# Kernel tuning notes

Measured on AMD Instinct MI355X. Metric: run time of the kernel, lower is better.

The kernel has to match this reference:

```python
import jax, jax.numpy as jnp
import numpy as np

# LIFParameters(thr=0.4, tau=20.0, tau_o=20.0, damp=0.3, n_ref=5)
THR = 0.4
DECAY = float(np.exp(-1.0 / 20.0))   # membrane decay
KAPPA = float(np.exp(-1.0 / 20.0))   # output filter decay
N_REF = 5.0
DAMP = 0.3
SCALE = 1.0                           # scaling_factor

B, NIN, H, NOUT = 1024, 2048, 2048, 512


def setup_inputs() -> dict:
    key = jax.random.key(0)
    ks = jax.random.split(key, 10)
    inputs = (jax.random.uniform(ks[0], (B, NIN)) < 0.1).astype(jnp.float32)   # input spikes
    v = jax.random.uniform(ks[1], (B, H)) * THR                                # membrane potentials
    z = (jax.random.uniform(ks[2], (B, H)) < 0.2).astype(jnp.float32)          # previous spikes
    r = jax.random.randint(ks[3], (B, H), 0, 6).astype(jnp.float32)            # refractory counters
    out = jax.random.normal(ks[4], (B, NOUT)) * 0.1                            # filtered output
    trace_in = jax.random.uniform(ks[5], (B, NIN))
    trace_rec = jax.random.uniform(ks[6], (B, H))
    w_in = jax.random.normal(ks[7], (NIN, H)) / np.sqrt(NIN)
    w_rec = jax.random.normal(ks[8], (H, H)) / np.sqrt(H)
    w_out = jax.random.normal(ks[9], (H, NOUT)) / np.sqrt(H)
    return dict(inputs=inputs, v=v, z=z, r=r, out=out, trace_in=trace_in,
                trace_rec=trace_rec, w_in=w_in, w_rec=w_rec, w_out=w_out)


@jax.custom_vjp
def spike(v_scaled):
    return (v_scaled > 0.0).astype(v_scaled.dtype)

def _spike_fwd(v_scaled):
    return spike(v_scaled), v_scaled

def _spike_bwd(v_scaled, g):
    # surrogate gradient: damp * max(0, 1 - |v_scaled|)
    return (g * DAMP * jnp.maximum(1.0 - jnp.abs(v_scaled), 0.0),)

spike.defvjp(_spike_fwd, _spike_bwd)


def reference(inputs, v, z, r, out, trace_in, trace_rec, w_in, w_rec, w_out):
    # --- lif_step ---
    i_t = inputs @ w_in + z @ w_rec                      # [B,H] synaptic current
    new_v = DECAY * v + i_t - z * THR                    # leaky integration + reset
    v_scaled = (new_v - THR) / THR
    new_z = spike(v_scaled)
    new_z = jnp.where(r > 0.1, 0.0, new_z)               # refractory masking (old r)
    new_r = jnp.clip(r + N_REF * new_z - 1.0, 0.0, N_REF)
    new_out = KAPPA * out + new_z @ (w_out * SCALE)      # [B,NOUT]
    # --- e-prop extras (call_eprop) ---
    dz_dh = jnp.maximum(DAMP * (1.0 - jnp.abs(v_scaled)), 0.0) / THR
    dz_dh = jnp.where(r > 0.1, 0.0, dz_dh)               # zero in refractory period
    new_trace_in = trace_in * DECAY + inputs
    new_trace_rec = trace_rec * DECAY + z
    return (new_out, new_z, new_v, new_r, new_trace_in, new_trace_rec, dz_dh)
```

## Files before the change

### kernel.cpp

```cpp
#include <hip/hip_runtime.h>

#define Bq 1024
#define Hq 2048
#define NOUTq 512

#define DECAYF 0.95122942450071400910f
#define THRF 0.4f
#define SINVF 5931641.0f

#define OFF_OUT  0
#define OFF_Z    524288
#define OFF_V    2621440
#define OFF_R    4718592
#define OFF_TIN  6815744
#define OFF_TREC 8912896
#define OFF_DZ   11010048

#define WS_A     0ul
#define WS_Q0    4194304ul
#define WS_Q1    12582912ul
#define WS_Q2    20971520ul
#define WS_WOUTT 29360128ul
#define WS_P     31457280ul
#define WS_Z2    65011712ul
#define WS_NEED  69206016ul

typedef __attribute__((ext_vector_type(8))) short  bf16x8;
typedef __attribute__((ext_vector_type(4))) short  s16x4;
typedef __attribute__((ext_vector_type(4))) float  f32x4;
typedef __attribute__((ext_vector_type(4))) int    i32x4;
typedef __attribute__((ext_vector_type(4))) char   c8x4;

#define VMCNT8  asm volatile("s_waitcnt vmcnt(8)" ::: "memory")
#define VMCNT0  asm volatile("s_waitcnt vmcnt(0)" ::: "memory")
#define LGKM0   asm volatile("s_waitcnt lgkmcnt(0)" ::: "memory")
#define SB0     __builtin_amdgcn_sched_barrier(0)
#define BARRAW  __builtin_amdgcn_s_barrier()

__device__ __forceinline__ unsigned short cvt_bf16(float f) {
  unsigned u = __float_as_uint(f);
  return (unsigned short)((u + 0x7FFFu + ((u >> 16) & 1u)) >> 16);
}

__device__ __forceinline__ void gl_lds16(const void* g, void* l) {
  __builtin_amdgcn_global_load_lds((const __attribute__((address_space(1))) unsigned int*)g,
                                   (__attribute__((address_space(3))) unsigned int*)l, 16, 0, 0);
}


__global__ __launch_bounds__(256)
void prep(const float* __restrict__ w_in, const float* __restrict__ w_rec,
          const float* __restrict__ w_out, signed char* __restrict__ Q0,
          signed char* __restrict__ Q1, signed char* __restrict__ Q2,
          short* __restrict__ WoutT,
          const f32x4* __restrict__ ins, const f32x4* __restrict__ zin,
          signed char* __restrict__ Acomb)
{
  __shared__ float tile[64][65];
  const int bx = blockIdx.x, tid = threadIdx.x;
  if (bx >= 2304) {
    const int i = (bx - 2304) * 256 + tid;
    const f32x4 b = ins[i];
    const f32x4 d = zin[i];
    const int e = i * 4, m = e >> 11, k = e & 2047;
    c8x4 ab, zb;
#pragma unroll
    for (int j = 0; j < 4; ++j) { ab[j] = (char)(b[j] != 0.0f); zb[j] = (char)(d[j] != 0.0f); }
    *(c8x4*)&Acomb[m * 4096 + k] = ab;
    *(c8x4*)&Acomb[m * 4096 + 2048 + k] = zb;
    return;
  }
  const int rr = tid >> 4, c4 = (tid & 15) * 4;
  if (bx < 2048) {
    const int k0 = (bx >> 5) * 64, n0 = (bx & 31) * 64;
#pragma unroll
    for (int p = 0; p < 4; ++p) {
      const int kk = p * 16 + rr, kg = k0 + kk;
      const float* src = (kg < 2048) ? &w_in[kg * 2048 + n0 + c4]
                                     : &w_rec[(kg - 2048) * 2048 + n0 + c4];
      const f32x4 v = *(const f32x4*)src;
#pragma unroll
      for (int j = 0; j < 4; ++j) tile[kk][c4 + j] = v[j];
    }
    __syncthreads();
#pragma unroll
    for (int p = 0; p < 4; ++p) {
      const int nn = p * 16 + rr;
      c8x4 b0, b1, b2;
#pragma unroll
      for (int j = 0; j < 4; ++j) {
        int q = __float2int_rn(tile[c4 + j][nn] * SINVF);
        const int d2 = ((q + 64) & 127) - 64;  q = (q - d2) >> 7;
        const int d1 = ((q + 64) & 127) - 64;  q = (q - d1) >> 7;
        b2[j] = (char)d2; b1[j] = (char)d1; b0[j] = (char)q;
      }
      const long off = (long)(n0 + nn) * 4096 + k0 + c4;
      *(c8x4*)&Q0[off] = b0;
      *(c8x4*)&Q1[off] = b1;
      *(c8x4*)&Q2[off] = b2;
    }
  } else {
    const int b2 = bx - 2048;
    const int k0 = (b2 >> 3) * 64, n0 = (b2 & 7) * 64;
#pragma unroll
    for (int p = 0; p < 4; ++p) {
      const int kk = p * 16 + rr;
      const f32x4 v = *(const f32x4*)&w_out[(k0 + kk) * 512 + n0 + c4];
#pragma unroll
      for (int j = 0; j < 4; ++j) tile[kk][c4 + j] = v[j];
    }
    __syncthreads();
#pragma unroll
    for (int p = 0; p < 4; ++p) {
      const int nn = p * 16 + rr;
      s16x4 hh;
#pragma unroll
      for (int j = 0; j < 4; ++j) hh[j] = (short)cvt_bf16(tile[c4 + j][nn]);
      *(s16x4*)&WoutT[(n0 + nn) * 2048 + k0 + c4] = hh;
    }
  }
}

__global__ __launch_bounds__(512, 1)
void gemm1(const signed char* __restrict__ Ag, const signed char* __restrict__ Q0g,
           const signed char* __restrict__ Q1g, const signed char* __restrict__ Q2g,
           int* __restrict__ outp)
{
  constexpr int KT = 8;
  __shared__ __align__(16) signed char L[2][4][16384];

  const int tid = threadIdx.x, lane = tid & 63, wv = tid >> 6;
  const int lr = lane & 15, hl = lane >> 4;
  const int r8 = lane >> 3, ts = lane & 7;

  const int bid = blockIdx.x;
  const int swz = (bid & 7) * 64 + (bid >> 3);
  const int m0 = (swz & 7) * 128;
  const int n0 = ((swz >> 3) & 15) * 128;
  const int kz = swz >> 7;
  const int kb = kz * 1024;
  int* P = outp + (size_t)kz * (Bq * Hq);

  const int wm = (wv & 3) * 32;
  const int wn = (wv >> 2) * 64;

  i32x4 a0[2][4], a1[2][4], a2[2][4];
#pragma unroll
  for (int mi = 0; mi < 2; ++mi)
#pragma unroll
    for (int ni = 0; ni < 4; ++ni) {
      a0[mi][ni] = (i32x4){0, 0, 0, 0};
      a1[mi][ni] = (i32x4){0, 0, 0, 0};
      a2[mi][ni] = (i32x4){0, 0, 0, 0};
    }

  auto STAGE = [&](int kt, int c) {
    const int k = kb + kt * 128;
#pragma unroll
    for (int q = 0; q < 2; ++q) {
      const int slot = wv * 2 + q;
      const int r = slot * 8 + r8;
      const int s = ts ^ (r & 7);
      const size_t go = (size_t)r * 4096 + k + s * 16;
      gl_lds16(Ag  + (size_t)m0 * 4096 + go, &L[c][0][slot * 1024]);
      gl_lds16(Q0g + (size_t)n0 * 4096 + go, &L[c][1][slot * 1024]);
      gl_lds16(Q1g + (size_t)n0 * 4096 + go, &L[c][2][slot * 1024]);
      gl_lds16(Q2g + (size_t)n0 * 4096 + go, &L[c][3][slot * 1024]);
    }
  };

  auto COMPUTE = [&](int c) {
#pragma unroll
    for (int ks = 0; ks < 2; ++ks) {
      i32x4 af[2];
#pragma unroll
      for (int mi = 0; mi < 2; ++mi) {
        const int ar = wm + mi * 16 + lr;
        af[mi] = *(const i32x4*)&L[c][0][ar * 128 + (((ks * 4 + hl) ^ (ar & 7)) << 4)];
      }
#pragma unroll
      for (int ni = 0; ni < 4; ++ni) {
        const int br = wn + ni * 16 + lr;
        const int sp = br * 128 + (((ks * 4 + hl) ^ (br & 7)) << 4);
        const i32x4 b0 = *(const i32x4*)&L[c][1][sp];
#pragma unroll
        for (int mi = 0; mi < 2; ++mi)
          a0[mi][ni] = __builtin_amdgcn_mfma_i32_16x16x64_i8(af[mi], b0, a0[mi][ni], 0, 0, 0);
        const i32x4 b1 = *(const i32x4*)&L[c][2][sp];
#pragma unroll
        for (int mi = 0; mi < 2; ++mi)
          a1[mi][ni] = __builtin_amdgcn_mfma_i32_16x16x64_i8(af[mi], b1, a1[mi][ni], 0, 0, 0);
        const i32x4 b2 = *(const i32x4*)&L[c][3][sp];
#pragma unroll
        for (int mi = 0; mi < 2; ++mi)
          a2[mi][ni] = __builtin_amdgcn_mfma_i32_16x16x64_i8(af[mi], b2, a2[mi][ni], 0, 0, 0);
      }
    }
  };

  STAGE(0, 0);
  STAGE(1, 1);
  for (int kt = 0; kt < KT - 1; ++kt) {
    VMCNT8; SB0; BARRAW; SB0;
    COMPUTE(kt & 1);
    LGKM0; SB0; BARRAW; SB0;
    if (kt + 2 < KT) STAGE(kt + 2, kt & 1);
  }
  VMCNT0; SB0; BARRAW; SB0;
  COMPUTE((KT - 1) & 1);

#pragma unroll
  for (int mi = 0; mi < 2; ++mi)
#pragma unroll
    for (int ni = 0; ni < 4; ++ni)
#pragma unroll
      for (int j = 0; j < 4; ++j) {
        const int m = m0 + wm + mi * 16 + hl * 4 + j;
        const int n = n0 + wn + ni * 16 + lr;
        P[m * Hq + n] = (a0[mi][ni][j] << 14) + (a1[mi][ni][j] << 7) + a2[mi][ni][j];
      }
}

__global__ __launch_bounds__(256)
void lif_epi(const i32x4* __restrict__ Pp, const f32x4* __restrict__ vin,
             const f32x4* __restrict__ zin, const f32x4* __restrict__ rin,
             float* __restrict__ dout, short* __restrict__ z2)
{
  const int i = blockIdx.x * 256 + threadIdx.x;
  const i32x4 c = Pp[i] + Pp[i + 524288] + Pp[i + 2 * 524288] + Pp[i + 3 * 524288];
  const double S = 1.0 / (double)SINVF;
  const f32x4 vo = vin[i], zo = zin[i], ro = rin[i];
  f32x4 nv, nz, nr, dz;
  s16x4 zb;
#pragma unroll
  for (int j = 0; j < 4; ++j) {
    const float it = (float)((double)c[j] * S);
    const float v1 = DECAYF * vo[j] + it - zo[j] * THRF;
    const float vs = (v1 - THRF) / THRF;
    const bool refr = ro[j] > 0.1f;
    const float z1 = (refr || !(vs > 0.0f)) ? 0.0f : 1.0f;
    nv[j] = v1; nz[j] = z1;
    nr[j] = fminf(fmaxf(ro[j] + 5.0f * z1 - 1.0f, 0.0f), 5.0f);
    dz[j] = refr ? 0.0f : (fmaxf(0.3f * (1.0f - fabsf(vs)), 0.0f) / THRF);
    zb[j] = (short)cvt_bf16(z1);
  }
  ((f32x4*)(dout + OFF_V))[i] = nv;
  ((f32x4*)(dout + OFF_Z))[i] = nz;
  ((f32x4*)(dout + OFF_R))[i] = nr;
  ((f32x4*)(dout + OFF_DZ))[i] = dz;
  ((s16x4*)z2)[i] = zb;
}

__global__ __launch_bounds__(256)
void tail(const short* __restrict__ Ag, const short* __restrict__ Whg,
          const float* __restrict__ e0, float* __restrict__ outp,
          const f32x4* __restrict__ tin, const f32x4* __restrict__ ins,
          const f32x4* __restrict__ trec, const f32x4* __restrict__ zin,
          f32x4* __restrict__ o1, f32x4* __restrict__ o2)
{
  constexpr int BM = 32, BN = 64, MR = 1, NR = 2, KT = 32, AK = 2048;
  constexpr int APW = BM / 32, WPW = BN / 32;
  __shared__ __align__(16) short As[BM * 64];
  __shared__ __align__(16) short Wh[BN * 64];

  const int bid = blockIdx.x, tid = threadIdx.x;
  if (bid >= 256) {
    const int i = (bid - 256) * 256 + tid;
    o1[i] = tin[i] * DECAYF + ins[i];
    o2[i] = trec[i] * DECAYF + zin[i];
    return;
  }
  const int lane = tid & 63, wv = tid >> 6;
  const int lr = lane & 15, hl = lane >> 4;
  const int rA = lane >> 3, ts = lane & 7;
  const int m0 = (bid >> 3) * BM, n0 = (bid & 7) * BN;
  const int wm = (wv >> 1) * (MR * 16);
  const int wn = (wv & 1) * (NR * 16);

  f32x4 acc[MR][NR];
#pragma unroll
  for (int mi = 0; mi < MR; ++mi)
#pragma unroll
    for (int ni = 0; ni < NR; ++ni) acc[mi][ni] = (f32x4){0.f, 0.f, 0.f, 0.f};

  auto STAGE = [&](int kt) {
    const int k = kt * 64;
#pragma unroll
    for (int q = 0; q < APW; ++q) {
      const int slot = wv * APW + q;
      const int r = slot * 8 + rA;
      const int s = ts ^ (r & 7);
      gl_lds16(Ag + (m0 + r) * AK + k + s * 8, &As[slot * 512]);
    }
#pragma unroll
    for (int q = 0; q < WPW; ++q) {
      const int slot = wv * WPW + q;
      const int r = slot * 8 + rA;
      const int s = ts ^ (r & 7);
      gl_lds16(Whg + (n0 + r) * AK + k + s * 8, &Wh[slot * 512]);
    }
  };

  STAGE(0);
  for (int kt = 0; kt < KT; ++kt) {
    __syncthreads();
#pragma unroll
    for (int ks = 0; ks < 2; ++ks) {
      bf16x8 af[MR];
#pragma unroll
      for (int mi = 0; mi < MR; ++mi) {
        const int r = wm + mi * 16 + lr;
        af[mi] = *(const bf16x8*)&As[r * 64 + (((ks * 4 + hl) ^ (r & 7)) << 3)];
      }
#pragma unroll
      for (int ni = 0; ni < NR; ++ni) {
        const int rn = wn + ni * 16 + lr;
        const int sp = (((ks * 4 + hl) ^ (rn & 7)) << 3);
        const bf16x8 bh = *(const bf16x8*)&Wh[rn * 64 + sp];
#pragma unroll
        for (int mi = 0; mi < MR; ++mi)
          acc[mi][ni] = __builtin_amdgcn_mfma_f32_16x16x32_bf16(af[mi], bh, acc[mi][ni], 0, 0, 0);
      }
    }
    __syncthreads();
    if (kt + 1 < KT) STAGE(kt + 1);
  }

#pragma unroll
  for (int mi = 0; mi < MR; ++mi)
#pragma unroll
    for (int ni = 0; ni < NR; ++ni)
#pragma unroll
      for (int j = 0; j < 4; ++j) {
        const int m = m0 + wm + mi * 16 + hl * 4 + j;
        const int n = n0 + wn + ni * 16 + lr;
        const int idx = m * NOUTq + n;
        outp[idx] = DECAYF * e0[idx] + acc[mi][ni][j];
      }
}


template<int MODE>
__global__ __launch_bounds__(256, 1)
void fb_gemm(const float* __restrict__ A0g, const float* __restrict__ A1g,
             const float* __restrict__ W0g, const float* __restrict__ W1g,
             const float* __restrict__ e0, const float* __restrict__ e1,
             const float* __restrict__ e2, float* __restrict__ dout)
{
  constexpr int BM = (MODE == 0) ? 64 : 32;
  constexpr int BN = (MODE == 0) ? 128 : 64;
  constexpr int BK = 64;
  constexpr int LDA = BK + 8;
  constexpr int MR = (MODE == 0) ? 2 : 1;
  constexpr int NR = (MODE == 0) ? 4 : 2;
  constexpr int WM = MR * 16, WN = NR * 16;
  constexpr int KT = (MODE == 0) ? 64 : 32;
  constexpr int Nmat = (MODE == 0) ? Hq : NOUTq;
  constexpr int QA = BM / 16;
  constexpr int QW = (16 * BN) / 256;
  constexpr int KSH = (MODE == 0) ? 7 : 6;
  constexpr int KSTEP = (MODE == 0) ? 2 : 4;

  __shared__ __align__(16) short As[BM * LDA];
  __shared__ __align__(16) short Wh[BN * LDA];
  __shared__ __align__(16) short Wl[((MODE == 0) ? BN : 1) * LDA];

  const int tid  = threadIdx.x;
  const int lane = tid & 63;
  const int wave = tid >> 6;
  const int lr = lane & 15, hl = lane >> 4;
  const int wmOff = (wave >> 1) * WM;
  const int wnOff = (wave & 1) * WN;
  const int m0 = blockIdx.y * BM;
  const int n0 = blockIdx.x * BN;
  const int arow = tid >> 4, ac4 = tid & 15;
  const int wn = tid & (BN - 1);

  f32x4 aR[QA];
  float wR[QW][4];
  f32x4 acc[MR][NR];
#pragma unroll
  for (int mi = 0; mi < MR; ++mi)
#pragma unroll
    for (int ni = 0; ni < NR; ++ni)
      acc[mi][ni] = (f32x4){0.f, 0.f, 0.f, 0.f};

  auto LOAD = [&](int kt) {
    const float* Ag = A0g; const float* Wg = W0g; int k0 = kt * BK;
    if (MODE == 0 && kt >= 32) { Ag = A1g; Wg = W1g; k0 = (kt - 32) * BK; }
#pragma unroll
    for (int q = 0; q < QA; ++q)
      aR[q] = *(const f32x4*)&Ag[(m0 + arow + q * 16) * 2048 + k0 + ac4 * 4];
#pragma unroll
    for (int p = 0; p < QW; ++p) {
      const int kq = (tid >> KSH) + p * KSTEP;
#pragma unroll
      for (int i = 0; i < 4; ++i)
        wR[p][i] = Wg[(k0 + kq * 4 + i) * Nmat + n0 + wn];
    }
  };

  auto STORE = [&]() {
#pragma unroll
    for (int q = 0; q < QA; ++q) {
      s16x4 hv;
#pragma unroll
      for (int j = 0; j < 4; ++j) hv[j] = (short)cvt_bf16(aR[q][j]);
      *(s16x4*)&As[(arow + q * 16) * LDA + ac4 * 4] = hv;
    }
#pragma unroll
    for (int p = 0; p < QW; ++p) {
      const int kq = (tid >> KSH) + p * KSTEP;
      s16x4 hh, ll;
#pragma unroll
      for (int i = 0; i < 4; ++i) {
        const float w = wR[p][i];
        const unsigned short h = cvt_bf16(w);
        hh[i] = (short)h;
        if (MODE == 0) {
          const float hf = __uint_as_float(((unsigned)h) << 16);
          ll[i] = (short)cvt_bf16(w - hf);
        }
      }
      *(s16x4*)&Wh[wn * LDA + kq * 4] = hh;
      if (MODE == 0) *(s16x4*)&Wl[wn * LDA + kq * 4] = ll;
    }
  };

  LOAD(0);
  for (int kt = 0; kt < KT; ++kt) {
    __syncthreads();
    STORE();
    __syncthreads();
    if (kt + 1 < KT) LOAD(kt + 1);
#pragma unroll
    for (int ks = 0; ks < 2; ++ks) {
      bf16x8 af[MR];
#pragma unroll
      for (int mi = 0; mi < MR; ++mi)
        af[mi] = *(const bf16x8*)&As[(wmOff + mi * 16 + lr) * LDA + ks * 32 + hl * 8];
#pragma unroll
      for (int ni = 0; ni < NR; ++ni) {
        const bf16x8 bh = *(const bf16x8*)&Wh[(wnOff + ni * 16 + lr) * LDA + ks * 32 + hl * 8];
#pragma unroll
        for (int mi = 0; mi < MR; ++mi)
          acc[mi][ni] = __builtin_amdgcn_mfma_f32_16x16x32_bf16(af[mi], bh, acc[mi][ni], 0, 0, 0);
        if (MODE == 0) {
          const bf16x8 bl = *(const bf16x8*)&Wl[(wnOff + ni * 16 + lr) * LDA + ks * 32 + hl * 8];
#pragma unroll
          for (int mi = 0; mi < MR; ++mi)
            acc[mi][ni] = __builtin_amdgcn_mfma_f32_16x16x32_bf16(af[mi], bl, acc[mi][ni], 0, 0, 0);
        }
      }
    }
  }

#pragma unroll
  for (int mi = 0; mi < MR; ++mi) {
#pragma unroll
    for (int ni = 0; ni < NR; ++ni) {
#pragma unroll
      for (int j = 0; j < 4; ++j) {
        const int m = m0 + wmOff + mi * 16 + hl * 4 + j;
        const int n = n0 + wnOff + ni * 16 + lr;
        if (MODE == 0) {
          const int idx = m * Hq + n;
          const float it = acc[mi][ni][j];
          const float vold = e0[idx];
          const float zold = e1[idx];
          const float rold = e2[idx];
          const float nv = DECAYF * vold + it - zold * THRF;
          const float vs = (nv - THRF) / THRF;
          const bool refr = rold > 0.1f;
          const float nz = (refr || !(vs > 0.0f)) ? 0.0f : 1.0f;
          const float nr = fminf(fmaxf(rold + 5.0f * nz - 1.0f, 0.0f), 5.0f);
          const float dz = refr ? 0.0f : (fmaxf(0.3f * (1.0f - fabsf(vs)), 0.0f) / THRF);
          dout[OFF_V + idx] = nv;
          dout[OFF_Z + idx] = nz;
          dout[OFF_R + idx] = nr;
          dout[OFF_DZ + idx] = dz;
        } else {
          const int idx = m * NOUTq + n;
          dout[OFF_OUT + idx] = DECAYF * e0[idx] + acc[mi][ni][j];
        }
      }
    }
  }
}

__global__ __launch_bounds__(256)
void fb_trace(const float4* __restrict__ tin, const float4* __restrict__ ins,
              const float4* __restrict__ trec, const float4* __restrict__ zin,
              float4* __restrict__ o1, float4* __restrict__ o2)
{
  const int n4 = (Bq * 2048) / 4;
  for (int i = blockIdx.x * blockDim.x + threadIdx.x; i < n4; i += gridDim.x * blockDim.x) {
    const float4 a = tin[i], b = ins[i];
    float4 u;
    u.x = a.x * DECAYF + b.x; u.y = a.y * DECAYF + b.y;
    u.z = a.z * DECAYF + b.z; u.w = a.w * DECAYF + b.w;
    o1[i] = u;
    const float4 c = trec[i], d = zin[i];
    float4 w;
    w.x = c.x * DECAYF + d.x; w.y = c.y * DECAYF + d.y;
    w.z = c.z * DECAYF + d.z; w.w = c.w * DECAYF + d.w;
    o2[i] = w;
  }
}

extern "C" void kernel_launch(void* const* d_in, const int* in_sizes, int n_in,
                              void* d_out, int out_size, void* d_ws, size_t ws_size,
                              hipStream_t stream) {
  const float* inputs = (const float*)d_in[0];
  const float* v      = (const float*)d_in[1];
  const float* z      = (const float*)d_in[2];
  const float* r      = (const float*)d_in[3];
  const float* outp   = (const float*)d_in[4];
  const float* tin    = (const float*)d_in[5];
  const float* trec   = (const float*)d_in[6];
  const float* w_in   = (const float*)d_in[7];
  const float* w_rec  = (const float*)d_in[8];
  const float* w_out  = (const float*)d_in[9];
  float* out = (float*)d_out;

  if (ws_size >= WS_NEED) {
    char* ws = (char*)d_ws;
    signed char* A  = (signed char*)(ws + WS_A);
    signed char* Q0 = (signed char*)(ws + WS_Q0);
    signed char* Q1 = (signed char*)(ws + WS_Q1);
    signed char* Q2 = (signed char*)(ws + WS_Q2);
    short* WoutT    = (short*)(ws + WS_WOUTT);
    int* P          = (int*)(ws + WS_P);
    short* Z2       = (short*)(ws + WS_Z2);

    prep<<<4352, 256, 0, stream>>>(w_in, w_rec, w_out, Q0, Q1, Q2, WoutT,
                                   (const f32x4*)inputs, (const f32x4*)z, A);
    gemm1<<<512, 512, 0, stream>>>(A, Q0, Q1, Q2, P);
    lif_epi<<<2048, 256, 0, stream>>>((const i32x4*)P, (const f32x4*)v, (const f32x4*)z,
                                      (const f32x4*)r, out, Z2);
    tail<<<2304, 256, 0, stream>>>(Z2, WoutT, outp, out + OFF_OUT,
                                   (const f32x4*)tin, (const f32x4*)inputs,
                                   (const f32x4*)trec, (const f32x4*)z,
                                   (f32x4*)(out + OFF_TIN), (f32x4*)(out + OFF_TREC));
  } else {
    fb_trace<<<2048, 256, 0, stream>>>((const float4*)tin, (const float4*)inputs,
                                       (const float4*)trec, (const float4*)z,
                                       (float4*)(out + OFF_TIN), (float4*)(out + OFF_TREC));
    fb_gemm<0><<<dim3(16, 16), 256, 0, stream>>>(inputs, z, w_in, w_rec, v, z, r, out);
    fb_gemm<1><<<dim3(8, 32), 256, 0, stream>>>(out + OFF_Z, nullptr, w_out, nullptr,
                                                outp, nullptr, nullptr, out);
  }
}
```

Measured before the change: 85.12 us.

## Retile int8 GEMM to 256x128 blocks with K-step 64 and 256 blocks

Changes the gemm1 block tile from 128x128 to 256x128 with a 64-wide K step, halving the grid to 256 blocks and giving each wave a 128x32 sub-tile. A-fragments are reused across more MFMAs and the B operand (three quantized weight slices) is loaded once per larger M tile, which cuts LDS and global traffic per MFMA. The LDS swizzle and wait counts are redone for the new layout. The cost is a larger accumulator footprint (48 i32x4 per thread), a grid of 256 blocks that may underfill the 256 CUs, and more loop iterations with barriers.

```diff
diff --git a/kernel.cpp b/kernel.cpp
--- a/kernel.cpp
+++ b/kernel.cpp
@@ -31,7 +31,7 @@
 typedef __attribute__((ext_vector_type(4))) int    i32x4;
 typedef __attribute__((ext_vector_type(4))) char   c8x4;
 
-#define VMCNT8  asm volatile("s_waitcnt vmcnt(8)" ::: "memory")
+#define VMCNT5  asm volatile("s_waitcnt vmcnt(5)" ::: "memory")
 #define VMCNT0  asm volatile("s_waitcnt vmcnt(0)" ::: "memory")
 #define LGKM0   asm volatile("s_waitcnt lgkmcnt(0)" ::: "memory")
 #define SB0     __builtin_amdgcn_sched_barrier(0)
@@ -126,82 +126,82 @@
            const signed char* __restrict__ Q1g, const signed char* __restrict__ Q2g,
            int* __restrict__ outp)
 {
-  constexpr int KT = 8;
-  __shared__ __align__(16) signed char L[2][4][16384];
+  constexpr int KT = 16;
+  __shared__ __align__(16) signed char As[2][16384];
+  __shared__ __align__(16) signed char Bs[2][3][8192];
 
   const int tid = threadIdx.x, lane = tid & 63, wv = tid >> 6;
   const int lr = lane & 15, hl = lane >> 4;
-  const int r8 = lane >> 3, ts = lane & 7;
+  const int r16 = lane >> 2, c4 = lane & 3;
+  const int gsw = c4 ^ ((r16 & 3) ^ ((r16 >> 2) & 3));
+  const int xv  = (lr & 3) ^ ((lr >> 2) & 3);
 
   const int bid = blockIdx.x;
-  const int swz = (bid & 7) * 64 + (bid >> 3);
-  const int m0 = (swz & 7) * 128;
-  const int n0 = ((swz >> 3) & 15) * 128;
-  const int kz = swz >> 7;
-  const int kb = kz * 1024;
+  const int swz = (bid & 7) * 32 + (bid >> 3);
+  const int kz  = swz >> 6;
+  const int tl  = swz & 63;
+  const int m0  = (tl & 3) * 256;
+  const int n0  = (tl >> 2) * 128;
+  const int kb  = kz * 1024;
   int* P = outp + (size_t)kz * (Bq * Hq);
 
-  const int wm = (wv & 3) * 32;
-  const int wn = (wv >> 2) * 64;
-
-  i32x4 a0[2][4], a1[2][4], a2[2][4];
-#pragma unroll
-  for (int mi = 0; mi < 2; ++mi)
-#pragma unroll
-    for (int ni = 0; ni < 4; ++ni) {
+  const int wm = (wv & 1) * 128;
+  const int wn = (wv >> 1) * 32;
+
+  i32x4 a0[8][2], a1[8][2], a2[8][2];
+#pragma unroll
+  for (int mi = 0; mi < 8; ++mi)
+#pragma unroll
+    for (int ni = 0; ni < 2; ++ni) {
       a0[mi][ni] = (i32x4){0, 0, 0, 0};
       a1[mi][ni] = (i32x4){0, 0, 0, 0};
       a2[mi][ni] = (i32x4){0, 0, 0, 0};
     }
 
   auto STAGE = [&](int kt, int c) {
-    const int k = kb + kt * 128;
+    const int k = kb + kt * 64;
 #pragma unroll
     for (int q = 0; q < 2; ++q) {
       const int slot = wv * 2 + q;
-      const int r = slot * 8 + r8;
-      const int s = ts ^ (r & 7);
-      const size_t go = (size_t)r * 4096 + k + s * 16;
-      gl_lds16(Ag  + (size_t)m0 * 4096 + go, &L[c][0][slot * 1024]);
-      gl_lds16(Q0g + (size_t)n0 * 4096 + go, &L[c][1][slot * 1024]);
-      gl_lds16(Q1g + (size_t)n0 * 4096 + go, &L[c][2][slot * 1024]);
-      gl_lds16(Q2g + (size_t)n0 * 4096 + go, &L[c][3][slot * 1024]);
+      gl_lds16(Ag + (size_t)(m0 + slot * 16 + r16) * 4096 + k + gsw * 16,
+               &As[c][slot * 1024]);
+    }
+    {
+      const int slot = wv;
+      const size_t go = (size_t)(n0 + slot * 16 + r16) * 4096 + k + gsw * 16;
+      gl_lds16(Q0g + go, &Bs[c][0][slot * 1024]);
+      gl_lds16(Q1g + go, &Bs[c][1][slot * 1024]);
+      gl_lds16(Q2g + go, &Bs[c][2][slot * 1024]);
     }
   };
 
   auto COMPUTE = [&](int c) {
-#pragma unroll
-    for (int ks = 0; ks < 2; ++ks) {
-      i32x4 af[2];
-#pragma unroll
-      for (int mi = 0; mi < 2; ++mi) {
-        const int ar = wm + mi * 16 + lr;
-        af[mi] = *(const i32x4*)&L[c][0][ar * 128 + (((ks * 4 + hl) ^ (ar & 7)) << 4)];
-      }
-#pragma unroll
-      for (int ni = 0; ni < 4; ++ni) {
-        const int br = wn + ni * 16 + lr;
-        const int sp = br * 128 + (((ks * 4 + hl) ^ (br & 7)) << 4);
-        const i32x4 b0 = *(const i32x4*)&L[c][1][sp];
-#pragma unroll
-        for (int mi = 0; mi < 2; ++mi)
-          a0[mi][ni] = __builtin_amdgcn_mfma_i32_16x16x64_i8(af[mi], b0, a0[mi][ni], 0, 0, 0);
-        const i32x4 b1 = *(const i32x4*)&L[c][2][sp];
-#pragma unroll
-        for (int mi = 0; mi < 2; ++mi)
-          a1[mi][ni] = __builtin_amdgcn_mfma_i32_16x16x64_i8(af[mi], b1, a1[mi][ni], 0, 0, 0);
-        const i32x4 b2 = *(const i32x4*)&L[c][3][sp];
-#pragma unroll
-        for (int mi = 0; mi < 2; ++mi)
-          a2[mi][ni] = __builtin_amdgcn_mfma_i32_16x16x64_i8(af[mi], b2, a2[mi][ni], 0, 0, 0);
-      }
+    i32x4 af[8];
+#pragma unroll
+    for (int mi = 0; mi < 8; ++mi)
+      af[mi] = *(const i32x4*)&As[c][(wm + mi * 16 + lr) * 64 + ((hl ^ xv) << 4)];
+#pragma unroll
+    for (int ni = 0; ni < 2; ++ni) {
+      const int boff = (wn + ni * 16 + lr) * 64 + ((hl ^ xv) << 4);
+      const i32x4 b0 = *(const i32x4*)&Bs[c][0][boff];
+#pragma unroll
+      for (int mi = 0; mi < 8; ++mi)
+        a0[mi][ni] = __builtin_amdgcn_mfma_i32_16x16x64_i8(af[mi], b0, a0[mi][ni], 0, 0, 0);
+      const i32x4 b1 = *(const i32x4*)&Bs[c][1][boff];
+#pragma unroll
+      for (int mi = 0; mi < 8; ++mi)
+        a1[mi][ni] = __builtin_amdgcn_mfma_i32_16x16x64_i8(af[mi], b1, a1[mi][ni], 0, 0, 0);
+      const i32x4 b2 = *(const i32x4*)&Bs[c][2][boff];
+#pragma unroll
+      for (int mi = 0; mi < 8; ++mi)
+        a2[mi][ni] = __builtin_amdgcn_mfma_i32_16x16x64_i8(af[mi], b2, a2[mi][ni], 0, 0, 0);
     }
   };
 
   STAGE(0, 0);
   STAGE(1, 1);
   for (int kt = 0; kt < KT - 1; ++kt) {
-    VMCNT8; SB0; BARRAW; SB0;
+    VMCNT5; SB0; BARRAW; SB0;
     COMPUTE(kt & 1);
     LGKM0; SB0; BARRAW; SB0;
     if (kt + 2 < KT) STAGE(kt + 2, kt & 1);
@@ -210,9 +210,9 @@
   COMPUTE((KT - 1) & 1);
 
 #pragma unroll
-  for (int mi = 0; mi < 2; ++mi)
-#pragma unroll
-    for (int ni = 0; ni < 4; ++ni)
+  for (int mi = 0; mi < 8; ++mi)
+#pragma unroll
+    for (int ni = 0; ni < 2; ++ni)
 #pragma unroll
       for (int j = 0; j < 4; ++j) {
         const int m = m0 + wm + mi * 16 + hl * 4 + j;
@@ -535,7 +535,7 @@
 
     prep<<<4352, 256, 0, stream>>>(w_in, w_rec, w_out, Q0, Q1, Q2, WoutT,
                                    (const f32x4*)inputs, (const f32x4*)z, A);
-    gemm1<<<512, 512, 0, stream>>>(A, Q0, Q1, Q2, P);
+    gemm1<<<256, 512, 0, stream>>>(A, Q0, Q1, Q2, P);
     lif_epi<<<2048, 256, 0, stream>>>((const i32x4*)P, (const f32x4*)v, (const f32x4*)z,
                                       (const f32x4*)r, out, Z2);
     tail<<<2304, 256, 0, stream>>>(Z2, WoutT, outp, out + OFF_OUT,
```

Result: slower. 90.57 us (+6.4%).
